# Optimization experiments

Measured on AMD Instinct MI355X. Metric: run time of the kernel, lower is better.

Reference implementation:

```python
import jax, jax.numpy as jnp
import numpy as np

D_MODEL = 1024


def setup_inputs() -> dict:
    key = jax.random.key(0)
    ks = jax.random.split(key, 9)
    d = D_MODEL
    s = 1.0 / np.sqrt(d)
    return {
        "x": jax.random.normal(ks[0], (4, 2048, d), dtype=jnp.float32),
        "w_q": jax.random.normal(ks[1], (d, d), dtype=jnp.float32) * s,
        "b_q": jnp.zeros((d,), dtype=jnp.float32),
        "w_k": jax.random.normal(ks[2], (d, d), dtype=jnp.float32) * s,
        "b_k": jnp.zeros((d,), dtype=jnp.float32),
        "w_v": jax.random.normal(ks[3], (d, d), dtype=jnp.float32) * s,
        "b_v": jnp.zeros((d,), dtype=jnp.float32),
        "w_out": jax.random.normal(ks[4], (d, d), dtype=jnp.float32) * s,
        "b_out": jnp.zeros((d,), dtype=jnp.float32),
    }


def reference(x, w_q, b_q, w_k, b_k, w_v, b_v, w_out, b_out):
    d_model = x.shape[-1]
    # torch Linear: y = x @ W^T + b
    Q = jnp.einsum("bsd,ed->bse", x, w_q) + b_q
    K = jnp.einsum("bsd,ed->bse", x, w_k) + b_k
    V = jnp.einsum("bsd,ed->bse", x, w_v) + b_v
    scores = jnp.einsum("bqd,bkd->bqk", Q, K) / jnp.sqrt(jnp.float32(d_model)).astype(x.dtype)
    attn = jax.nn.softmax(scores, axis=-1)
    out = jnp.einsum("bqk,bkd->bqd", attn, V)
    return jnp.einsum("bsd,ed->bse", out, w_out) + b_out
```

## Files before the change

### kernel.cpp

```cpp
#include <hip/hip_runtime.h>


typedef __bf16 bf16x8 __attribute__((ext_vector_type(8)));
typedef float f32x4 __attribute__((ext_vector_type(4)));

__device__ __forceinline__ unsigned short f32_to_bf16(float f) {
  unsigned int u = __float_as_uint(f);
  u += 0x7fffu + ((u >> 16) & 1u);
  return (unsigned short)(u >> 16);
}

__device__ __forceinline__ void load_lds16(const void* g, void* l) {
  __builtin_amdgcn_global_load_lds(
      (const __attribute__((address_space(1))) void*)g,
      (__attribute__((address_space(3))) void*)l, 16, 0, 0);
}

__global__ __launch_bounds__(256) void cast_f32_bf16(
    const float4* __restrict__ in, ushort4* __restrict__ out, int n4) {
  int i = blockIdx.x * 256 + threadIdx.x;
  if (i < n4) {
    float4 f = in[i];
    ushort4 u;
    u.x = f32_to_bf16(f.x);
    u.y = f32_to_bf16(f.y);
    u.z = f32_to_bf16(f.z);
    u.w = f32_to_bf16(f.w);
    out[i] = u;
  }
}

__global__ __launch_bounds__(256) void gemm_bt(
    const unsigned short* __restrict__ A, const unsigned short* __restrict__ B,
    void* __restrict__ C, const float* __restrict__ bias,
    int M, int N, int K, float alpha, int out_bf16,
    long long sA, long long sB, long long sC) {
  __shared__ unsigned short As[128 * 64];
  __shared__ unsigned short Bs[128 * 64];

  const int bz = blockIdx.z;
  A += (long long)bz * sA;
  B += (long long)bz * sB;

  const int bm = blockIdx.y, bn = blockIdx.x;
  const int tid = threadIdx.x;
  const int lane = tid & 63, wave = tid >> 6;
  const int wr = wave >> 1, wc = wave & 1;
  const int l16 = lane & 15, quad = lane >> 4;

  f32x4 acc[4][4] = {};

  const int srow = tid >> 3;
  const int xr = srow & 7;
  const int scol = ((tid & 7) ^ xr) * 8;
  const unsigned short* gA = A + (long long)(bm * 128 + srow) * K + scol;
  const unsigned short* gB = B + (long long)(bn * 128 + srow) * K + scol;
  char* ldsA = (char*)As + wave * 1024;
  char* ldsB = (char*)Bs + wave * 1024;

  for (int k0 = 0; k0 < K; k0 += 64) {
#pragma unroll
    for (int r = 0; r < 4; r++)
      load_lds16(gA + k0 + (long long)r * 32 * K, ldsA + r * 4096);
#pragma unroll
    for (int r = 0; r < 4; r++)
      load_lds16(gB + k0 + (long long)r * 32 * K, ldsB + r * 4096);
    __syncthreads();

    const int swz = l16 & 7;
#pragma unroll
    for (int kk = 0; kk < 64; kk += 32) {
      bf16x8 af[4], bf[4];
      const int lc = (kk >> 3) + quad;
      const int pco = (lc ^ swz) * 8;
#pragma unroll
      for (int mi = 0; mi < 4; mi++)
        af[mi] = *(const bf16x8*)(As + (wr * 64 + mi * 16 + l16) * 64 + pco);
#pragma unroll
      for (int ni = 0; ni < 4; ni++)
        bf[ni] = *(const bf16x8*)(Bs + (wc * 64 + ni * 16 + l16) * 64 + pco);
#pragma unroll
      for (int mi = 0; mi < 4; mi++)
#pragma unroll
        for (int ni = 0; ni < 4; ni++)
          acc[mi][ni] = __builtin_amdgcn_mfma_f32_16x16x32_bf16(
              af[mi], bf[ni], acc[mi][ni], 0, 0, 0);
    }
    __syncthreads();
  }

  const int orow0 = bm * 128 + wr * 64 + quad * 4;
  const int ocol0 = bn * 128 + wc * 64 + l16;
  if (out_bf16) {
    unsigned short* Cp = (unsigned short*)C + (long long)bz * sC;
#pragma unroll
    for (int mi = 0; mi < 4; mi++)
#pragma unroll
      for (int ni = 0; ni < 4; ni++) {
        const int col = ocol0 + ni * 16;
        const float bv = bias ? bias[col] : 0.f;
#pragma unroll
        for (int r = 0; r < 4; r++) {
          const float o = acc[mi][ni][r] * alpha + bv;
          Cp[(long long)(orow0 + mi * 16 + r) * N + col] = f32_to_bf16(o);
        }
      }
  } else {
    float* Cp = (float*)C + (long long)bz * sC;
#pragma unroll
    for (int mi = 0; mi < 4; mi++)
#pragma unroll
      for (int ni = 0; ni < 4; ni++) {
        const int col = ocol0 + ni * 16;
        const float bv = bias ? bias[col] : 0.f;
#pragma unroll
        for (int r = 0; r < 4; r++) {
          const float o = acc[mi][ni][r] * alpha + bv;
          Cp[(long long)(orow0 + mi * 16 + r) * N + col] = o;
        }
      }
  }
}

__global__ __launch_bounds__(256) void transpose_v(
    const unsigned short* __restrict__ V, unsigned short* __restrict__ VT) {
  __shared__ unsigned short tile[64][65];
  const int d0 = blockIdx.x * 64, s0 = blockIdx.y * 64, b = blockIdx.z;
  const int t = threadIdx.x;
  const unsigned short* src = V + ((long long)b * 2048 + s0) * 1024 + d0;
#pragma unroll
  for (int i = 0; i < 16; i++) {
    int lin = t + i * 256;
    int r = lin >> 6, c = lin & 63;
    tile[r][c] = src[(long long)r * 1024 + c];
  }
  __syncthreads();
  unsigned short* dst = VT + ((long long)b * 1024 + d0) * 2048 + s0;
#pragma unroll
  for (int i = 0; i < 16; i++) {
    int lin = t + i * 256;
    int r = lin >> 6, c = lin & 63;
    dst[(long long)r * 2048 + c] = tile[c][r];
  }
}

__global__ __launch_bounds__(256) void softmax_rows(
    const float* __restrict__ S, unsigned short* __restrict__ P) {
  const long long row = blockIdx.x;
  const float* s = S + row * 2048;
  const int t = threadIdx.x;
  float v[8];
  float mx = -3.4e38f;
#pragma unroll
  for (int i = 0; i < 8; i++) {
    v[i] = s[t + i * 256];
    mx = fmaxf(mx, v[i]);
  }
#pragma unroll
  for (int o = 32; o >= 1; o >>= 1) mx = fmaxf(mx, __shfl_xor(mx, o));
  __shared__ float red[4], red2[4];
  if ((t & 63) == 0) red[t >> 6] = mx;
  __syncthreads();
  mx = fmaxf(fmaxf(red[0], red[1]), fmaxf(red[2], red[3]));
  float sum = 0.f;
#pragma unroll
  for (int i = 0; i < 8; i++) {
    v[i] = __expf(v[i] - mx);
    sum += v[i];
  }
#pragma unroll
  for (int o = 32; o >= 1; o >>= 1) sum += __shfl_xor(sum, o);
  if ((t & 63) == 0) red2[t >> 6] = sum;
  __syncthreads();
  sum = red2[0] + red2[1] + red2[2] + red2[3];
  const float inv = 1.0f / sum;
  unsigned short* p = P + row * 2048;
#pragma unroll
  for (int i = 0; i < 8; i++) p[t + i * 256] = f32_to_bf16(v[i] * inv);
}

extern "C" void kernel_launch(void* const* d_in, const int* in_sizes, int n_in,
                              void* d_out, int out_size, void* d_ws,
                              size_t ws_size, hipStream_t stream) {
  const float* x = (const float*)d_in[0];
  const float* wq = (const float*)d_in[1];
  const float* bq = (const float*)d_in[2];
  const float* wk = (const float*)d_in[3];
  const float* bk = (const float*)d_in[4];
  const float* wv = (const float*)d_in[5];
  const float* bv = (const float*)d_in[6];
  const float* wo = (const float*)d_in[7];
  const float* bo = (const float*)d_in[8];
  float* out = (float*)d_out;
  char* ws = (char*)d_ws;
  const size_t MB = 1ull << 20;

  unsigned short* xb  = (unsigned short*)(ws + 0);
  unsigned short* wqb = (unsigned short*)(ws + 16 * MB);
  unsigned short* wkb = (unsigned short*)(ws + 18 * MB);
  unsigned short* wvb = (unsigned short*)(ws + 20 * MB);
  unsigned short* wob = (unsigned short*)(ws + 22 * MB);
  unsigned short* Q   = (unsigned short*)(ws + 24 * MB);
  unsigned short* Kb  = (unsigned short*)(ws + 40 * MB);
  unsigned short* VT  = (unsigned short*)(ws + 56 * MB);
  unsigned short* V   = (unsigned short*)(ws + 72 * MB);
  float*          S   = (float*)(ws + 72 * MB);
  unsigned short* P   = Q;
  unsigned short* O   = xb;

  cast_f32_bf16<<<dim3(8192), dim3(256), 0, stream>>>((const float4*)x,
                                                      (ushort4*)xb, 2097152);
  cast_f32_bf16<<<dim3(1024), dim3(256), 0, stream>>>((const float4*)wq,
                                                      (ushort4*)wqb, 262144);
  cast_f32_bf16<<<dim3(1024), dim3(256), 0, stream>>>((const float4*)wk,
                                                      (ushort4*)wkb, 262144);
  cast_f32_bf16<<<dim3(1024), dim3(256), 0, stream>>>((const float4*)wv,
                                                      (ushort4*)wvb, 262144);
  cast_f32_bf16<<<dim3(1024), dim3(256), 0, stream>>>((const float4*)wo,
                                                      (ushort4*)wob, 262144);

  gemm_bt<<<dim3(8, 64, 1), dim3(256), 0, stream>>>(xb, wqb, Q, bq, 8192, 1024,
                                                    1024, 1.f, 1, 0, 0, 0);
  gemm_bt<<<dim3(8, 64, 1), dim3(256), 0, stream>>>(xb, wkb, Kb, bk, 8192, 1024,
                                                    1024, 1.f, 1, 0, 0, 0);
  gemm_bt<<<dim3(8, 64, 1), dim3(256), 0, stream>>>(xb, wvb, V, bv, 8192, 1024,
                                                    1024, 1.f, 1, 0, 0, 0);

  transpose_v<<<dim3(16, 32, 4), dim3(256), 0, stream>>>(V, VT);

  gemm_bt<<<dim3(16, 16, 4), dim3(256), 0, stream>>>(
      Q, Kb, S, nullptr, 2048, 2048, 1024, 0.03125f, 0, 2048ll * 1024,
      2048ll * 1024, 2048ll * 2048);

  softmax_rows<<<dim3(8192), dim3(256), 0, stream>>>(S, P);

  gemm_bt<<<dim3(8, 16, 4), dim3(256), 0, stream>>>(
      P, VT, O, nullptr, 2048, 1024, 2048, 1.f, 1, 2048ll * 2048, 1024ll * 2048,
      2048ll * 1024);

  gemm_bt<<<dim3(8, 64, 1), dim3(256), 0, stream>>>(O, wob, out, bo, 8192, 1024,
                                                    1024, 1.f, 0, 0, 0, 0);
}
```

Baseline: 342.1 us.

## Fuse Q/K projections, compute V transposed directly, store scores as bf16

Concatenates the Q and K weights and biases so a single GEMM produces both projections into one strided buffer. V^T is produced directly by computing W_v·x^T per batch with a row-bias mode, which removes the separate transpose kernel. Attention scores are written as bf16 instead of fp32, and softmax runs in place with vectorized 16-byte loads and stores. The four weight casts are merged into one launch. Together these cut launches and memory traffic, at the cost of rounding the scores to bf16 before softmax and adding leading-dimension and bias-mode parameters to the GEMM.

```diff
diff --git a/kernel.cpp b/kernel.cpp
--- a/kernel.cpp
+++ b/kernel.cpp
@@ -3,11 +3,16 @@
 
 typedef __bf16 bf16x8 __attribute__((ext_vector_type(8)));
 typedef float f32x4 __attribute__((ext_vector_type(4)));
+typedef unsigned short ushort8 __attribute__((ext_vector_type(8)));
 
 __device__ __forceinline__ unsigned short f32_to_bf16(float f) {
   unsigned int u = __float_as_uint(f);
   u += 0x7fffu + ((u >> 16) & 1u);
   return (unsigned short)(u >> 16);
+}
+
+__device__ __forceinline__ float bf16_to_f32(unsigned short u) {
+  return __uint_as_float((unsigned int)u << 16);
 }
 
 __device__ __forceinline__ void load_lds16(const void* g, void* l) {
@@ -30,10 +35,39 @@
   }
 }
 
+__global__ __launch_bounds__(256) void cast_weights(
+    const float4* __restrict__ wq, const float4* __restrict__ wk,
+    const float4* __restrict__ wv, const float4* __restrict__ wo,
+    ushort4* __restrict__ wqkb, ushort4* __restrict__ wvb,
+    ushort4* __restrict__ wob) {
+  const int b = blockIdx.x;
+  const int seg = b >> 10;
+  const int idx = ((b & 1023) << 8) + threadIdx.x;
+  const float4* src = seg == 0 ? wq : seg == 1 ? wk : seg == 2 ? wv : wo;
+  ushort4* dst = seg == 0 ? wqkb
+               : seg == 1 ? (wqkb + 262144)
+               : seg == 2 ? wvb : wob;
+  float4 f = src[idx];
+  ushort4 u;
+  u.x = f32_to_bf16(f.x);
+  u.y = f32_to_bf16(f.y);
+  u.z = f32_to_bf16(f.z);
+  u.w = f32_to_bf16(f.w);
+  dst[idx] = u;
+}
+
+__global__ __launch_bounds__(256) void concat_bias(
+    const float* __restrict__ bq, const float* __restrict__ bk,
+    float* __restrict__ bqk) {
+  int i = blockIdx.x * 256 + threadIdx.x;
+  bqk[i] = (i < 1024) ? bq[i] : bk[i - 1024];
+}
+
 __global__ __launch_bounds__(256) void gemm_bt(
     const unsigned short* __restrict__ A, const unsigned short* __restrict__ B,
     void* __restrict__ C, const float* __restrict__ bias,
-    int M, int N, int K, float alpha, int out_bf16,
+    int M, int N, int K, int ldA, int ldB, int ldC,
+    float alpha, int out_bf16, int bias_mode,
     long long sA, long long sB, long long sC) {
   __shared__ unsigned short As[128 * 64];
   __shared__ unsigned short Bs[128 * 64];
@@ -53,18 +87,18 @@
   const int srow = tid >> 3;
   const int xr = srow & 7;
   const int scol = ((tid & 7) ^ xr) * 8;
-  const unsigned short* gA = A + (long long)(bm * 128 + srow) * K + scol;
-  const unsigned short* gB = B + (long long)(bn * 128 + srow) * K + scol;
+  const unsigned short* gA = A + (long long)(bm * 128 + srow) * ldA + scol;
+  const unsigned short* gB = B + (long long)(bn * 128 + srow) * ldB + scol;
   char* ldsA = (char*)As + wave * 1024;
   char* ldsB = (char*)Bs + wave * 1024;
 
   for (int k0 = 0; k0 < K; k0 += 64) {
 #pragma unroll
     for (int r = 0; r < 4; r++)
-      load_lds16(gA + k0 + (long long)r * 32 * K, ldsA + r * 4096);
+      load_lds16(gA + k0 + (long long)r * 32 * ldA, ldsA + r * 4096);
 #pragma unroll
     for (int r = 0; r < 4; r++)
-      load_lds16(gB + k0 + (long long)r * 32 * K, ldsB + r * 4096);
+      load_lds16(gB + k0 + (long long)r * 32 * ldB, ldsB + r * 4096);
     __syncthreads();
 
     const int swz = l16 & 7;
@@ -98,11 +132,13 @@
 #pragma unroll
       for (int ni = 0; ni < 4; ni++) {
         const int col = ocol0 + ni * 16;
-        const float bv = bias ? bias[col] : 0.f;
+        const float cb = (bias_mode == 1) ? bias[col] : 0.f;
 #pragma unroll
         for (int r = 0; r < 4; r++) {
+          const int row = orow0 + mi * 16 + r;
+          const float bv = (bias_mode == 2) ? bias[row] : cb;
           const float o = acc[mi][ni][r] * alpha + bv;
-          Cp[(long long)(orow0 + mi * 16 + r) * N + col] = f32_to_bf16(o);
+          Cp[(long long)row * ldC + col] = f32_to_bf16(o);
         }
       }
   } else {
@@ -112,48 +148,29 @@
 #pragma unroll
       for (int ni = 0; ni < 4; ni++) {
         const int col = ocol0 + ni * 16;
-        const float bv = bias ? bias[col] : 0.f;
+        const float cb = (bias_mode == 1) ? bias[col] : 0.f;
 #pragma unroll
         for (int r = 0; r < 4; r++) {
+          const int row = orow0 + mi * 16 + r;
+          const float bv = (bias_mode == 2) ? bias[row] : cb;
           const float o = acc[mi][ni][r] * alpha + bv;
-          Cp[(long long)(orow0 + mi * 16 + r) * N + col] = o;
+          Cp[(long long)row * ldC + col] = o;
         }
       }
   }
 }
 
-__global__ __launch_bounds__(256) void transpose_v(
-    const unsigned short* __restrict__ V, unsigned short* __restrict__ VT) {
-  __shared__ unsigned short tile[64][65];
-  const int d0 = blockIdx.x * 64, s0 = blockIdx.y * 64, b = blockIdx.z;
+__global__ __launch_bounds__(256) void softmax_rows_bf16(
+    unsigned short* __restrict__ S) {
+  const long long row = blockIdx.x;
+  unsigned short* s = S + row * 2048;
   const int t = threadIdx.x;
-  const unsigned short* src = V + ((long long)b * 2048 + s0) * 1024 + d0;
-#pragma unroll
-  for (int i = 0; i < 16; i++) {
-    int lin = t + i * 256;
-    int r = lin >> 6, c = lin & 63;
-    tile[r][c] = src[(long long)r * 1024 + c];
-  }
-  __syncthreads();
-  unsigned short* dst = VT + ((long long)b * 1024 + d0) * 2048 + s0;
-#pragma unroll
-  for (int i = 0; i < 16; i++) {
-    int lin = t + i * 256;
-    int r = lin >> 6, c = lin & 63;
-    dst[(long long)r * 2048 + c] = tile[c][r];
-  }
-}
-
-__global__ __launch_bounds__(256) void softmax_rows(
-    const float* __restrict__ S, unsigned short* __restrict__ P) {
-  const long long row = blockIdx.x;
-  const float* s = S + row * 2048;
-  const int t = threadIdx.x;
+  ushort8 u = *(const ushort8*)(s + t * 8);
   float v[8];
   float mx = -3.4e38f;
 #pragma unroll
   for (int i = 0; i < 8; i++) {
-    v[i] = s[t + i * 256];
+    v[i] = bf16_to_f32(u[i]);
     mx = fmaxf(mx, v[i]);
   }
 #pragma unroll
@@ -174,9 +191,10 @@
   __syncthreads();
   sum = red2[0] + red2[1] + red2[2] + red2[3];
   const float inv = 1.0f / sum;
-  unsigned short* p = P + row * 2048;
-#pragma unroll
-  for (int i = 0; i < 8; i++) p[t + i * 256] = f32_to_bf16(v[i] * inv);
+  ushort8 w;
+#pragma unroll
+  for (int i = 0; i < 8; i++) w[i] = f32_to_bf16(v[i] * inv);
+  *(ushort8*)(s + t * 8) = w;
 }
 
 extern "C" void kernel_launch(void* const* d_in, const int* in_sizes, int n_in,
@@ -195,49 +213,41 @@
   char* ws = (char*)d_ws;
   const size_t MB = 1ull << 20;
 
-  unsigned short* xb  = (unsigned short*)(ws + 0);
-  unsigned short* wqb = (unsigned short*)(ws + 16 * MB);
-  unsigned short* wkb = (unsigned short*)(ws + 18 * MB);
-  unsigned short* wvb = (unsigned short*)(ws + 20 * MB);
-  unsigned short* wob = (unsigned short*)(ws + 22 * MB);
-  unsigned short* Q   = (unsigned short*)(ws + 24 * MB);
-  unsigned short* Kb  = (unsigned short*)(ws + 40 * MB);
-  unsigned short* VT  = (unsigned short*)(ws + 56 * MB);
-  unsigned short* V   = (unsigned short*)(ws + 72 * MB);
-  float*          S   = (float*)(ws + 72 * MB);
-  unsigned short* P   = Q;
-  unsigned short* O   = xb;
+  unsigned short* xb   = (unsigned short*)(ws + 0);
+  unsigned short* wqkb = (unsigned short*)(ws + 16 * MB);
+  unsigned short* wvb  = (unsigned short*)(ws + 20 * MB);
+  unsigned short* wob  = (unsigned short*)(ws + 22 * MB);
+  unsigned short* QK   = (unsigned short*)(ws + 24 * MB);
+  unsigned short* VT   = (unsigned short*)(ws + 56 * MB);
+  unsigned short* S    = (unsigned short*)(ws + 72 * MB);
+  float*          bqk  = (float*)(ws + 104 * MB);
+  unsigned short* O    = xb;
 
   cast_f32_bf16<<<dim3(8192), dim3(256), 0, stream>>>((const float4*)x,
                                                       (ushort4*)xb, 2097152);
-  cast_f32_bf16<<<dim3(1024), dim3(256), 0, stream>>>((const float4*)wq,
-                                                      (ushort4*)wqb, 262144);
-  cast_f32_bf16<<<dim3(1024), dim3(256), 0, stream>>>((const float4*)wk,
-                                                      (ushort4*)wkb, 262144);
-  cast_f32_bf16<<<dim3(1024), dim3(256), 0, stream>>>((const float4*)wv,
-                                                      (ushort4*)wvb, 262144);
-  cast_f32_bf16<<<dim3(1024), dim3(256), 0, stream>>>((const float4*)wo,
-                                                      (ushort4*)wob, 262144);
-
-  gemm_bt<<<dim3(8, 64, 1), dim3(256), 0, stream>>>(xb, wqb, Q, bq, 8192, 1024,
-                                                    1024, 1.f, 1, 0, 0, 0);
-  gemm_bt<<<dim3(8, 64, 1), dim3(256), 0, stream>>>(xb, wkb, Kb, bk, 8192, 1024,
-                                                    1024, 1.f, 1, 0, 0, 0);
-  gemm_bt<<<dim3(8, 64, 1), dim3(256), 0, stream>>>(xb, wvb, V, bv, 8192, 1024,
-                                                    1024, 1.f, 1, 0, 0, 0);
-
-  transpose_v<<<dim3(16, 32, 4), dim3(256), 0, stream>>>(V, VT);
+  cast_weights<<<dim3(4096), dim3(256), 0, stream>>>(
+      (const float4*)wq, (const float4*)wk, (const float4*)wv,
+      (const float4*)wo, (ushort4*)wqkb, (ushort4*)wvb, (ushort4*)wob);
+  concat_bias<<<dim3(8), dim3(256), 0, stream>>>(bq, bk, bqk);
+
+  gemm_bt<<<dim3(16, 64, 1), dim3(256), 0, stream>>>(
+      xb, wqkb, QK, bqk, 8192, 2048, 1024, 1024, 1024, 2048, 1.f, 1, 1, 0, 0,
+      0);
+
+  gemm_bt<<<dim3(16, 8, 4), dim3(256), 0, stream>>>(
+      wvb, xb, VT, bv, 1024, 2048, 1024, 1024, 1024, 2048, 1.f, 1, 2, 0,
+      2048ll * 1024, 1024ll * 2048);
 
   gemm_bt<<<dim3(16, 16, 4), dim3(256), 0, stream>>>(
-      Q, Kb, S, nullptr, 2048, 2048, 1024, 0.03125f, 0, 2048ll * 1024,
-      2048ll * 1024, 2048ll * 2048);
-
-  softmax_rows<<<dim3(8192), dim3(256), 0, stream>>>(S, P);
+      QK, QK + 1024, S, nullptr, 2048, 2048, 1024, 2048, 2048, 2048, 0.03125f,
+      1, 0, 2048ll * 2048, 2048ll * 2048, 2048ll * 2048);
+
+  softmax_rows_bf16<<<dim3(8192), dim3(256), 0, stream>>>(S);
 
   gemm_bt<<<dim3(8, 16, 4), dim3(256), 0, stream>>>(
-      P, VT, O, nullptr, 2048, 1024, 2048, 1.f, 1, 2048ll * 2048, 1024ll * 2048,
-      2048ll * 1024);
-
-  gemm_bt<<<dim3(8, 64, 1), dim3(256), 0, stream>>>(O, wob, out, bo, 8192, 1024,
-                                                    1024, 1.f, 0, 0, 0, 0);
-}
+      S, VT, O, nullptr, 2048, 1024, 2048, 2048, 2048, 1024, 1.f, 1, 0,
+      2048ll * 2048, 1024ll * 2048, 2048ll * 1024);
+
+  gemm_bt<<<dim3(8, 64, 1), dim3(256), 0, stream>>>(
+      O, wob, out, bo, 8192, 1024, 1024, 1024, 1024, 1024, 1.f, 0, 1, 0, 0, 0);
+}
```

After: 351.1 us. 1.03x slower.
